# Kernel tuning notes

Measured on AMD Instinct MI355X. Metric: run time of the kernel, lower is better.

The kernel has to match this reference:

```python
import jax, jax.numpy as jnp
import numpy as np

D_MODEL = 1024
NUM_HEADS = 16
D_K = D_MODEL // NUM_HEADS


def setup_inputs() -> dict:
    key = jax.random.key(0)
    ks = jax.random.split(key, 12)
    B, S = 2, 2048
    s = 1.0 / np.sqrt(D_MODEL)
    return {
        "query": jax.random.normal(ks[0], (B, S, D_MODEL), jnp.float32),
        "key": jax.random.normal(ks[1], (B, S, D_MODEL), jnp.float32),
        "value": jax.random.normal(ks[2], (B, S, D_MODEL), jnp.float32),
        "w_q": jax.random.normal(ks[3], (D_MODEL, D_MODEL), jnp.float32) * s,
        "b_q": jnp.zeros((D_MODEL,), jnp.float32),
        "w_k": jax.random.normal(ks[4], (D_MODEL, D_MODEL), jnp.float32) * s,
        "b_k": jnp.zeros((D_MODEL,), jnp.float32),
        "w_v": jax.random.normal(ks[5], (D_MODEL, D_MODEL), jnp.float32) * s,
        "b_v": jnp.zeros((D_MODEL,), jnp.float32),
        "w_o": jax.random.normal(ks[6], (D_MODEL, D_MODEL), jnp.float32) * s,
        "b_o": jnp.zeros((D_MODEL,), jnp.float32),
    }


def reference(query, key, value, w_q, b_q, w_k, b_k, w_v, b_v, w_o, b_o):
    B, S, _ = query.shape
    H, Dk = NUM_HEADS, D_K
    # Linear projections (torch Linear: x @ W.T + b), split into heads -> [B,H,S,Dk]
    q = (query @ w_q.T + b_q).reshape(B, S, H, Dk).transpose(0, 2, 1, 3)
    k = (key @ w_k.T + b_k).reshape(B, -1, H, Dk).transpose(0, 2, 1, 3)
    v = (value @ w_v.T + b_v).reshape(B, -1, H, Dk).transpose(0, 2, 1, 3)
    # Scaled dot-product attention
    scores = jnp.einsum("bhqd,bhkd->bhqk", q, k) / jnp.sqrt(jnp.asarray(Dk, q.dtype))
    attn = jax.nn.softmax(scores, axis=-1)
    x = jnp.einsum("bhqk,bhkd->bhqd", attn, v)
    # Merge heads and output projection
    x = x.transpose(0, 2, 1, 3).reshape(B, S, H * Dk)
    return x @ w_o.T + b_o
```

## Files before the change

### kernel.cpp

```cpp
#include <hip/hip_runtime.h>
#include <hip/hip_fp16.h>
#include <stdint.h>

#define S_LEN 2048
#define BATCH 2
#define NHEAD 16
#define DKH 64
#define DMODEL 1024
#define MTOT (BATCH * S_LEN)
#define NT (S_LEN / 64)

#define QSCALE 0.18033688011112042f
#define M2F 8.65617024533378f

typedef _Float16 h16;
typedef __attribute__((ext_vector_type(8))) _Float16 f16x8;
typedef __attribute__((ext_vector_type(4))) _Float16 f16x4;
typedef __attribute__((ext_vector_type(4))) float f32x4;

union F8 { unsigned int u[4]; f16x8 v; };

__device__ __forceinline__ h16 f2h(float f) { return (h16)f; }

__device__ __forceinline__ float fexp2(float x) {
    float r;
    asm("v_exp_f32 %0, %1" : "=v"(r) : "v"(x));
    return r;
}

__device__ __forceinline__ f16x8 gload16(const h16* p) {
    f16x8 r;
    asm volatile("global_load_dwordx4 %0, %1, off" : "=v"(r) : "v"(p));
    return r;
}

typedef __attribute__((address_space(1))) void GV;
typedef __attribute__((address_space(3))) void LV;
__device__ __forceinline__ void load_lds16(const h16* g, h16* l) {
    __builtin_amdgcn_global_load_lds((GV*)g, (LV*)l, 16, 0, 0);
}

__global__ void cvt_all(const float* __restrict__ q, const float* __restrict__ k,
                        const float* __restrict__ v, const float* __restrict__ wq,
                        const float* __restrict__ wk, const float* __restrict__ wv,
                        const float* __restrict__ wo,
                        h16* __restrict__ Xq, h16* __restrict__ Xk, h16* __restrict__ Xv,
                        h16* __restrict__ Wq, h16* __restrict__ Wk, h16* __restrict__ Wv,
                        h16* __restrict__ Wo) {
    const size_t i4 = ((size_t)blockIdx.x * 256 + threadIdx.x) * 4;
    const float* s;
    h16* d;
    size_t off;
    if (i4 < (3ull << 22)) {
        const int t = (int)(i4 >> 22);
        off = i4 & ((1ull << 22) - 1);
        s = t == 0 ? q : t == 1 ? k : v;
        d = t == 0 ? Xq : t == 1 ? Xk : Xv;
    } else {
        const size_t j = i4 - (3ull << 22);
        const int t = (int)(j >> 20);
        off = j & ((1ull << 20) - 1);
        s = t == 0 ? wq : t == 1 ? wk : t == 2 ? wv : wo;
        d = t == 0 ? Wq : t == 1 ? Wk : t == 2 ? Wv : Wo;
    }
    const float4 val = *(const float4*)(s + off);
    f16x4 o = { (h16)val.x, (h16)val.y, (h16)val.z, (h16)val.w };
    *(f16x4*)(d + off) = o;
}

template <int MODE>
__device__ __forceinline__ void gemm_body(const h16* __restrict__ A,
                                          const h16* __restrict__ W,
                                          const float* __restrict__ bias,
                                          void* __restrict__ out, float scale,
                                          int bm, int bn,
                                          h16 (*lA)[128 * 32], h16 (*lB)[128 * 32]) {
    constexpr int K = DMODEL;
    const int tid = threadIdx.x;
    const int lane = tid & 63, wid = tid >> 6;
    const int g = lane >> 4, lr = lane & 15;
    const int wr = wid >> 1, wc = wid & 1;

    const h16* Ap = A + (size_t)(bm + wid * 16 + (lane >> 2)) * K + (lane & 3) * 8;
    const h16* Wp = W + (size_t)(bn + wid * 16 + (lane >> 2)) * K + (lane & 3) * 8;
    const int ldst = wid * 16 * 32 + lane * 8;

    f32x4 acc[4][4] = {};

    load_lds16(Ap,          &lA[0][ldst]);
    load_lds16(Ap + 64 * K, &lA[0][64 * 32 + ldst]);
    load_lds16(Wp,          &lB[0][ldst]);
    load_lds16(Wp + 64 * K, &lB[0][64 * 32 + ldst]);
    __syncthreads();

    int cur = 0;
    for (int k0 = 0; k0 < K; k0 += 32) {
        if (k0 + 32 < K) {
            load_lds16(Ap + k0 + 32,          &lA[cur ^ 1][ldst]);
            load_lds16(Ap + 64 * K + k0 + 32, &lA[cur ^ 1][64 * 32 + ldst]);
            load_lds16(Wp + k0 + 32,          &lB[cur ^ 1][ldst]);
            load_lds16(Wp + 64 * K + k0 + 32, &lB[cur ^ 1][64 * 32 + ldst]);
        }
        f16x8 af[4], bf[4];
#pragma unroll
        for (int i = 0; i < 4; ++i) {
            af[i] = *(const f16x8*)&lA[cur][(wr * 64 + i * 16 + lr) * 32 + g * 8];
            bf[i] = *(const f16x8*)&lB[cur][(wc * 64 + i * 16 + lr) * 32 + g * 8];
        }
#pragma unroll
        for (int i = 0; i < 4; ++i)
#pragma unroll
            for (int j = 0; j < 4; ++j)
                acc[i][j] = __builtin_amdgcn_mfma_f32_16x16x32_f16(af[i], bf[j], acc[i][j], 0, 0, 0);
        __syncthreads();
        cur ^= 1;
    }

#pragma unroll
    for (int i = 0; i < 4; ++i) {
        const int row0 = bm + wr * 64 + i * 16 + g * 4;
#pragma unroll
        for (int j = 0; j < 4; ++j) {
            const int col = bn + wc * 64 + j * 16 + lr;
            const float bv = bias[col];
            f32x4 v = acc[i][j];
            if constexpr (MODE == 2) {
                float* o = (float*)out;
#pragma unroll
                for (int r = 0; r < 4; ++r) o[(size_t)(row0 + r) * DMODEL + col] = v[r] + bv;
            } else {
                const int b = row0 >> 11, s0 = row0 & (S_LEN - 1);
                const int h = col >> 6, d = col & 63;
                h16* o = (h16*)out;
                if constexpr (MODE == 0) {
                    size_t base = ((size_t)(b * NHEAD + h) * S_LEN + s0) * DKH + d;
#pragma unroll
                    for (int r = 0; r < 4; ++r)
                        o[base + (size_t)r * DKH] = f2h((v[r] + bv) * scale);
                } else {
                    size_t base = ((size_t)(b * NHEAD + h) * DKH + d) * S_LEN + s0;
                    f16x4 pk = { f2h(v[0] + bv), f2h(v[1] + bv), f2h(v[2] + bv), f2h(v[3] + bv) };
                    *(f16x4*)&o[base] = pk;
                }
            }
        }
    }
}

__global__ __launch_bounds__(256) void gemm_qkv(
        const h16* __restrict__ Xq, const h16* __restrict__ Xk, const h16* __restrict__ Xv,
        const h16* __restrict__ Wq, const h16* __restrict__ Wk, const h16* __restrict__ Wv,
        const float* __restrict__ bq, const float* __restrict__ bk, const float* __restrict__ bv,
        h16* __restrict__ Qp, h16* __restrict__ Kp, h16* __restrict__ Vt) {
    __shared__ h16 lA[2][128 * 32];
    __shared__ h16 lB[2][128 * 32];
    const int bm = blockIdx.x * 128, bn = blockIdx.y * 128;
    const int which = blockIdx.z;
    if (which == 0)
        gemm_body<0>(Xq, Wq, bq, Qp, QSCALE, bm, bn, lA, lB);
    else if (which == 1)
        gemm_body<0>(Xk, Wk, bk, Kp, 1.0f, bm, bn, lA, lB);
    else
        gemm_body<1>(Xv, Wv, bv, Vt, 1.0f, bm, bn, lA, lB);
}

__global__ __launch_bounds__(256) void gemm_o(const h16* __restrict__ A,
                                              const h16* __restrict__ W,
                                              const float* __restrict__ bias,
                                              float* __restrict__ out) {
    __shared__ h16 lA[2][128 * 32];
    __shared__ h16 lB[2][128 * 32];
    gemm_body<2>(A, W, bias, out, 1.0f, blockIdx.x * 128, blockIdx.y * 128, lA, lB);
}

__device__ __forceinline__ void stage_k(const h16* __restrict__ Kh, int kv0,
                                        h16* ldsK, int wid, int lane) {
    const int rbase = wid * 16;
#pragma unroll
    for (int i = 0; i < 2; ++i) {
        const int row = rbase + i * 8 + (lane >> 3);
        const int cbs = ((lane & 7) * 16) ^ ((row & 7) << 4);
        load_lds16(Kh + (size_t)(kv0 + row) * DKH + (cbs >> 1),
                   ldsK + (rbase + i * 8) * DKH + lane * 8);
    }
}

__device__ __forceinline__ void vload(const h16* __restrict__ Vh, int kv0,
                                      int g, int lr, f16x8 (&vr)[8]) {
#pragma unroll
    for (int ks = 0; ks < 2; ++ks)
#pragma unroll
        for (int mf = 0; mf < 4; ++mf)
            vr[ks * 4 + mf] = gload16(&Vh[(size_t)(mf * 16 + lr) * S_LEN + kv0 + ks * 32 + g * 8]);
}

__device__ __forceinline__ void fa_tile(const h16* __restrict__ Kh,
                                        const h16* __restrict__ Vh, int kvn,
                                        const h16* lK, h16* lKn,
                                        char* pb, int sw,
                                        const f16x8 (&qf)[2][2],
                                        const f16x8 (&vc)[8], f16x8 (&vn)[8],
                                        f32x4 (&cacc)[2][4], f32x4 (&lsum)[2],
                                        int g, int lr, int wid, int lane) {
    stage_k(Kh, kvn, lKn, wid, lane);
    vload(Vh, kvn, g, lr, vn);

    f16x8 kf[8];
#pragma unroll
    for (int ks = 0; ks < 2; ++ks)
#pragma unroll
        for (int mf = 0; mf < 4; ++mf) {
            const int cbs = (ks * 64 + g * 16) ^ ((lr & 7) << 4);
            kf[ks * 4 + mf] = *(const f16x8*)&lK[(mf * 16 + lr) * DKH + (cbs >> 1)];
        }

#pragma unroll
    for (int qg = 0; qg < 2; ++qg) {
        f32x4 sa[4];
#pragma unroll
        for (int mf = 0; mf < 4; ++mf) sa[mf] = (f32x4){-M2F, -M2F, -M2F, -M2F};
        __builtin_amdgcn_s_setprio(1);
#pragma unroll
        for (int ks = 0; ks < 2; ++ks)
#pragma unroll
            for (int mf = 0; mf < 4; ++mf)
                sa[mf] = __builtin_amdgcn_mfma_f32_16x16x32_f16(kf[ks * 4 + mf], qf[qg][ks], sa[mf], 0, 0, 0);
        __builtin_amdgcn_s_setprio(0);

#pragma unroll
        for (int mf = 0; mf < 4; ++mf)
#pragma unroll
            for (int r = 0; r < 4; ++r)
                sa[mf][r] = fexp2(sa[mf][r]);
#pragma unroll
        for (int mf = 0; mf < 4; ++mf) lsum[qg] += sa[mf];

#pragma unroll
        for (int mf = 0; mf < 4; ++mf) {
            unsigned int p0 = __builtin_bit_cast(unsigned int, __builtin_amdgcn_cvt_pkrtz(sa[mf][0], sa[mf][1]));
            unsigned int p1 = __builtin_bit_cast(unsigned int, __builtin_amdgcn_cvt_pkrtz(sa[mf][2], sa[mf][3]));
            *(uint64_t*)(pb + ((mf * 32 + g * 8) ^ sw)) = (uint64_t)p0 | ((uint64_t)p1 << 32);
        }
#pragma unroll
        for (int ks = 0; ks < 2; ++ks) {
            F8 pf;
            pf.v = *(const f16x8*)(pb + ((ks * 64 + g * 16) ^ sw));
            __builtin_amdgcn_s_setprio(1);
#pragma unroll
            for (int mf = 0; mf < 4; ++mf)
                cacc[qg][mf] = __builtin_amdgcn_mfma_f32_16x16x32_f16(vc[ks * 4 + mf], pf.v, cacc[qg][mf], 0, 0, 0);
            __builtin_amdgcn_s_setprio(0);
        }
    }

    asm volatile("s_waitcnt vmcnt(0)");
    __syncthreads();
}

__global__ __launch_bounds__(256, 2) void flash_attn(const h16* __restrict__ Q,
                                                     const h16* __restrict__ Kp,
                                                     const h16* __restrict__ Vt,
                                                     h16* __restrict__ ctx) {
    const int tid = threadIdx.x;
    const int lane = tid & 63, wid = tid >> 6;
    const int g = lane >> 4, lr = lane & 15;
    const int wg = blockIdx.x;
    const int swz = (wg & 7) * 64 + (wg >> 3);
    const int bh = swz >> 4;
    const int qbase = (swz & 15) * 128 + wid * 32;

    __shared__ h16 ldsK[2][64 * DKH];
    __shared__ __align__(16) char ldsP[4][2048];

    const h16* Qh = Q + (size_t)bh * S_LEN * DKH;
    const h16* Kh = Kp + (size_t)bh * S_LEN * DKH;
    const h16* Vh = Vt + (size_t)bh * DKH * S_LEN;

    f16x8 qf[2][2];
#pragma unroll
    for (int qg = 0; qg < 2; ++qg)
#pragma unroll
        for (int ks = 0; ks < 2; ++ks)
            qf[qg][ks] = *(const f16x8*)&Qh[(size_t)(qbase + qg * 16 + lr) * DKH + ks * 32 + g * 8];

    char* pb = &ldsP[wid][lr * 128];
    const int sw = (lr & 7) << 4;

    f32x4 cacc[2][4] = {};
    f32x4 lsum[2] = {};

    f16x8 vA[8], vB[8];
    stage_k(Kh, 0, ldsK[0], wid, lane);
    vload(Vh, 0, g, lr, vA);
    asm volatile("s_waitcnt vmcnt(0)");
    __syncthreads();

    for (int t = 0; t < NT; t += 2) {
        fa_tile(Kh, Vh, (t + 1) * 64, ldsK[0], ldsK[1], pb, sw, qf, vA, vB,
                cacc, lsum, g, lr, wid, lane);
        const int kv2 = (t + 2 < NT) ? (t + 2) * 64 : 0;
        fa_tile(Kh, Vh, kv2, ldsK[1], ldsK[0], pb, sw, qf, vB, vA,
                cacc, lsum, g, lr, wid, lane);
    }

    const int b = bh >> 4, h = bh & (NHEAD - 1);
#pragma unroll
    for (int qg = 0; qg < 2; ++qg) {
        float l = (lsum[qg][0] + lsum[qg][1]) + (lsum[qg][2] + lsum[qg][3]);
        l += __shfl_xor(l, 16);
        l += __shfl_xor(l, 32);
        const float inv = 1.f / l;
        const int qabs = qbase + qg * 16 + lr;
        h16* o = ctx + ((size_t)(b * S_LEN + qabs)) * DMODEL + h * DKH;
#pragma unroll
        for (int mf = 0; mf < 4; ++mf) {
            f16x4 st = { f2h(cacc[qg][mf][0] * inv), f2h(cacc[qg][mf][1] * inv),
                         f2h(cacc[qg][mf][2] * inv), f2h(cacc[qg][mf][3] * inv) };
            *(f16x4*)&o[mf * 16 + g * 4] = st;
        }
    }
}

extern "C" void kernel_launch(void* const* d_in, const int* in_sizes, int n_in,
                              void* d_out, int out_size, void* d_ws, size_t ws_size,
                              hipStream_t stream) {
    const float* q_in = (const float*)d_in[0];
    const float* k_in = (const float*)d_in[1];
    const float* v_in = (const float*)d_in[2];
    const float* w_q = (const float*)d_in[3];
    const float* b_q = (const float*)d_in[4];
    const float* w_k = (const float*)d_in[5];
    const float* b_k = (const float*)d_in[6];
    const float* w_v = (const float*)d_in[7];
    const float* b_v = (const float*)d_in[8];
    const float* w_o = (const float*)d_in[9];
    const float* b_o = (const float*)d_in[10];
    float* out = (float*)d_out;

    char* ws = (char*)d_ws;
    h16* Wq = (h16*)(ws + (0ull << 20));
    h16* Wk = (h16*)(ws + (2ull << 20));
    h16* Wv = (h16*)(ws + (4ull << 20));
    h16* Wo = (h16*)(ws + (6ull << 20));
    h16* Qp = (h16*)(ws + (8ull << 20));
    h16* Kp = (h16*)(ws + (16ull << 20));
    h16* Vt = (h16*)(ws + (24ull << 20));
    h16* Xv = (h16*)(ws + (32ull << 20));
    h16* ctx = Xv;
    h16* Xq = (h16*)d_out;
    h16* Xk = (h16*)((char*)d_out + (8ull << 20));

    cvt_all<<<dim3(16384), 256, 0, stream>>>(q_in, k_in, v_in, w_q, w_k, w_v, w_o,
                                             Xq, Xk, Xv, Wq, Wk, Wv, Wo);

    gemm_qkv<<<dim3(MTOT / 128, DMODEL / 128, 3), 256, 0, stream>>>(
        Xq, Xk, Xv, Wq, Wk, Wv, b_q, b_k, b_v, Qp, Kp, Vt);

    flash_attn<<<dim3(512), 256, 0, stream>>>(Qp, Kp, Vt, ctx);

    gemm_o<<<dim3(MTOT / 128, DMODEL / 128), 256, 0, stream>>>(ctx, Wo, b_o, out);
}
```

Before: 246.1 us.

## Stage V tiles through double-buffered LDS alongside K in flash attention

V tiles are now copied into a double-buffered LDS array with async global-to-LDS loads, using the same swizzle as K. Before, each wave loaded its own V fragments from global memory into registers. The change lets the four waves of a block share one global fetch of V per tile and frees the registers that held two V register sets. The tile loop is flattened from a manual two-step unroll into a single loop with a buffer index. The cost is more LDS capacity and LDS read traffic per tile. The explicit vmcnt wait before each barrier is also dropped, so correctness depends on the compiler inserting that wait for the LDS DMA loads.

```diff
diff --git a/kernel.cpp b/kernel.cpp
--- a/kernel.cpp
+++ b/kernel.cpp
@@ -25,12 +25,6 @@
 __device__ __forceinline__ float fexp2(float x) {
     float r;
     asm("v_exp_f32 %0, %1" : "=v"(r) : "v"(x));
-    return r;
-}
-
-__device__ __forceinline__ f16x8 gload16(const h16* p) {
-    f16x8 r;
-    asm volatile("global_load_dwordx4 %0, %1, off" : "=v"(r) : "v"(p));
     return r;
 }
 
@@ -173,8 +167,9 @@
     gemm_body<2>(A, W, bias, out, 1.0f, blockIdx.x * 128, blockIdx.y * 128, lA, lB);
 }
 
-__device__ __forceinline__ void stage_k(const h16* __restrict__ Kh, int kv0,
-                                        h16* ldsK, int wid, int lane) {
+__device__ __forceinline__ void stage_kv(const h16* __restrict__ Kh,
+                                         const h16* __restrict__ Vh, int kv0,
+                                         h16* ldsK, h16* ldsV, int wid, int lane) {
     const int rbase = wid * 16;
 #pragma unroll
     for (int i = 0; i < 2; ++i) {
@@ -182,79 +177,9 @@
         const int cbs = ((lane & 7) * 16) ^ ((row & 7) << 4);
         load_lds16(Kh + (size_t)(kv0 + row) * DKH + (cbs >> 1),
                    ldsK + (rbase + i * 8) * DKH + lane * 8);
-    }
-}
-
-__device__ __forceinline__ void vload(const h16* __restrict__ Vh, int kv0,
-                                      int g, int lr, f16x8 (&vr)[8]) {
-#pragma unroll
-    for (int ks = 0; ks < 2; ++ks)
-#pragma unroll
-        for (int mf = 0; mf < 4; ++mf)
-            vr[ks * 4 + mf] = gload16(&Vh[(size_t)(mf * 16 + lr) * S_LEN + kv0 + ks * 32 + g * 8]);
-}
-
-__device__ __forceinline__ void fa_tile(const h16* __restrict__ Kh,
-                                        const h16* __restrict__ Vh, int kvn,
-                                        const h16* lK, h16* lKn,
-                                        char* pb, int sw,
-                                        const f16x8 (&qf)[2][2],
-                                        const f16x8 (&vc)[8], f16x8 (&vn)[8],
-                                        f32x4 (&cacc)[2][4], f32x4 (&lsum)[2],
-                                        int g, int lr, int wid, int lane) {
-    stage_k(Kh, kvn, lKn, wid, lane);
-    vload(Vh, kvn, g, lr, vn);
-
-    f16x8 kf[8];
-#pragma unroll
-    for (int ks = 0; ks < 2; ++ks)
-#pragma unroll
-        for (int mf = 0; mf < 4; ++mf) {
-            const int cbs = (ks * 64 + g * 16) ^ ((lr & 7) << 4);
-            kf[ks * 4 + mf] = *(const f16x8*)&lK[(mf * 16 + lr) * DKH + (cbs >> 1)];
-        }
-
-#pragma unroll
-    for (int qg = 0; qg < 2; ++qg) {
-        f32x4 sa[4];
-#pragma unroll
-        for (int mf = 0; mf < 4; ++mf) sa[mf] = (f32x4){-M2F, -M2F, -M2F, -M2F};
-        __builtin_amdgcn_s_setprio(1);
-#pragma unroll
-        for (int ks = 0; ks < 2; ++ks)
-#pragma unroll
-            for (int mf = 0; mf < 4; ++mf)
-                sa[mf] = __builtin_amdgcn_mfma_f32_16x16x32_f16(kf[ks * 4 + mf], qf[qg][ks], sa[mf], 0, 0, 0);
-        __builtin_amdgcn_s_setprio(0);
-
-#pragma unroll
-        for (int mf = 0; mf < 4; ++mf)
-#pragma unroll
-            for (int r = 0; r < 4; ++r)
-                sa[mf][r] = fexp2(sa[mf][r]);
-#pragma unroll
-        for (int mf = 0; mf < 4; ++mf) lsum[qg] += sa[mf];
-
-#pragma unroll
-        for (int mf = 0; mf < 4; ++mf) {
-            unsigned int p0 = __builtin_bit_cast(unsigned int, __builtin_amdgcn_cvt_pkrtz(sa[mf][0], sa[mf][1]));
-            unsigned int p1 = __builtin_bit_cast(unsigned int, __builtin_amdgcn_cvt_pkrtz(sa[mf][2], sa[mf][3]));
-            *(uint64_t*)(pb + ((mf * 32 + g * 8) ^ sw)) = (uint64_t)p0 | ((uint64_t)p1 << 32);
-        }
-#pragma unroll
-        for (int ks = 0; ks < 2; ++ks) {
-            F8 pf;
-            pf.v = *(const f16x8*)(pb + ((ks * 64 + g * 16) ^ sw));
-            __builtin_amdgcn_s_setprio(1);
-#pragma unroll
-            for (int mf = 0; mf < 4; ++mf)
-                cacc[qg][mf] = __builtin_amdgcn_mfma_f32_16x16x32_f16(vc[ks * 4 + mf], pf.v, cacc[qg][mf], 0, 0, 0);
-            __builtin_amdgcn_s_setprio(0);
-        }
-    }
-
-    asm volatile("s_waitcnt vmcnt(0)");
-    __syncthreads();
+        load_lds16(Vh + (size_t)row * S_LEN + kv0 + (cbs >> 1),
+                   ldsV + (rbase + i * 8) * DKH + lane * 8);
+    }
 }
 
 __global__ __launch_bounds__(256, 2) void flash_attn(const h16* __restrict__ Q,
@@ -270,6 +195,7 @@
     const int qbase = (swz & 15) * 128 + wid * 32;
 
     __shared__ h16 ldsK[2][64 * DKH];
+    __shared__ h16 ldsV[2][64 * DKH];
     __shared__ __align__(16) char ldsP[4][2048];
 
     const h16* Qh = Q + (size_t)bh * S_LEN * DKH;
@@ -289,18 +215,70 @@
     f32x4 cacc[2][4] = {};
     f32x4 lsum[2] = {};
 
-    f16x8 vA[8], vB[8];
-    stage_k(Kh, 0, ldsK[0], wid, lane);
-    vload(Vh, 0, g, lr, vA);
-    asm volatile("s_waitcnt vmcnt(0)");
+    stage_kv(Kh, Vh, 0, ldsK[0], ldsV[0], wid, lane);
     __syncthreads();
 
-    for (int t = 0; t < NT; t += 2) {
-        fa_tile(Kh, Vh, (t + 1) * 64, ldsK[0], ldsK[1], pb, sw, qf, vA, vB,
-                cacc, lsum, g, lr, wid, lane);
-        const int kv2 = (t + 2 < NT) ? (t + 2) * 64 : 0;
-        fa_tile(Kh, Vh, kv2, ldsK[1], ldsK[0], pb, sw, qf, vB, vA,
-                cacc, lsum, g, lr, wid, lane);
+    int cur = 0;
+    for (int t = 0; t < NT; ++t) {
+        if (t + 1 < NT)
+            stage_kv(Kh, Vh, (t + 1) * 64, ldsK[cur ^ 1], ldsV[cur ^ 1], wid, lane);
+
+        const h16* lK = ldsK[cur];
+        const h16* lV = ldsV[cur];
+
+        f16x8 kf[8], vf[8];
+#pragma unroll
+        for (int ks = 0; ks < 2; ++ks)
+#pragma unroll
+            for (int mf = 0; mf < 4; ++mf) {
+                const int cbs = (ks * 64 + g * 16) ^ ((lr & 7) << 4);
+                kf[ks * 4 + mf] = *(const f16x8*)&lK[(mf * 16 + lr) * DKH + (cbs >> 1)];
+                vf[ks * 4 + mf] = *(const f16x8*)&lV[(mf * 16 + lr) * DKH + (cbs >> 1)];
+            }
+
+#pragma unroll
+        for (int qg = 0; qg < 2; ++qg) {
+            f32x4 sa[4];
+#pragma unroll
+            for (int mf = 0; mf < 4; ++mf) sa[mf] = (f32x4){-M2F, -M2F, -M2F, -M2F};
+            __builtin_amdgcn_s_setprio(1);
+#pragma unroll
+            for (int ks = 0; ks < 2; ++ks)
+#pragma unroll
+                for (int mf = 0; mf < 4; ++mf)
+                    sa[mf] = __builtin_amdgcn_mfma_f32_16x16x32_f16(kf[ks * 4 + mf], qf[qg][ks], sa[mf], 0, 0, 0);
+            __builtin_amdgcn_s_setprio(0);
+
+#pragma unroll
+            for (int mf = 0; mf < 4; ++mf)
+#pragma unroll
+                for (int r = 0; r < 4; ++r)
+                    sa[mf][r] = fexp2(sa[mf][r]);
+#pragma unroll
+            for (int mf = 0; mf < 4; ++mf) lsum[qg] += sa[mf];
+
+#pragma unroll
+            for (int mf = 0; mf < 4; ++mf) {
+                unsigned int p0 = __builtin_bit_cast(unsigned int, __builtin_amdgcn_cvt_pkrtz(sa[mf][0], sa[mf][1]));
+                unsigned int p1 = __builtin_bit_cast(unsigned int, __builtin_amdgcn_cvt_pkrtz(sa[mf][2], sa[mf][3]));
+                *(uint64_t*)(pb + ((mf * 32 + g * 8) ^ sw)) =
+                    (uint64_t)p0 | ((uint64_t)p1 << 32);
+            }
+
+#pragma unroll
+            for (int ks = 0; ks < 2; ++ks) {
+                F8 pf;
+                pf.v = *(const f16x8*)(pb + ((ks * 64 + g * 16) ^ sw));
+                __builtin_amdgcn_s_setprio(1);
+#pragma unroll
+                for (int mf = 0; mf < 4; ++mf)
+                    cacc[qg][mf] = __builtin_amdgcn_mfma_f32_16x16x32_f16(vf[ks * 4 + mf], pf.v, cacc[qg][mf], 0, 0, 0);
+                __builtin_amdgcn_s_setprio(0);
+            }
+        }
+
+        __syncthreads();
+        cur ^= 1;
     }
 
     const int b = bh >> 4, h = bh & (NHEAD - 1);
```

Result: faster. 221.0 us (-10.2%).
